# Kernel optimization log

Measured on AMD Instinct MI355X. Metric: run time of the kernel, lower is better.

## Reference

```python
import jax, jax.numpy as jnp
import numpy as np

THETA = 10000.0


def apply_rope(x, token_position, theta=THETA):
    # x: [B, H, S, d_k] with interleaved even/odd pairs; token_position: [B, S]
    B, H, S, d_k = x.shape
    inv_freq = 1.0 / theta ** (jnp.arange(0, d_k, 2, dtype=jnp.float32) / d_k)  # [d_k/2]
    angles = token_position.astype(jnp.float32)[:, :, None] * inv_freq[None, None, :]  # [B,S,d_k/2]
    cos = jnp.cos(angles)[:, None, :, :]  # [B,1,S,d_k/2]
    sin = jnp.sin(angles)[:, None, :, :]
    xp = x.reshape(B, H, S, d_k // 2, 2)
    x_even, x_odd = xp[..., 0], xp[..., 1]
    rot_even = x_even * cos - x_odd * sin
    rot_odd = x_even * sin + x_odd * cos
    return jnp.stack([rot_even, rot_odd], axis=-1).reshape(B, H, S, d_k)


def setup_inputs() -> dict:
    key = jax.random.key(0)
    ks = jax.random.split(key, 6)
    B, S, D = 2, 2048, 2048
    x = jax.random.normal(ks[0], (B, S, D), dtype=jnp.float32)
    token_position = jnp.sort(jax.random.randint(ks[1], (B, S), 0, 2048), axis=-1).astype(jnp.int32)
    scale = 0.02
    WQ = jax.random.normal(ks[2], (D, D), dtype=jnp.float32) * scale
    WK = jax.random.normal(ks[3], (D, D), dtype=jnp.float32) * scale
    WV = jax.random.normal(ks[4], (D, D), dtype=jnp.float32) * scale
    WO = jax.random.normal(ks[5], (D, D), dtype=jnp.float32) * scale
    return {"x": x, "token_position": token_position, "WQ": WQ, "WK": WK, "WV": WV, "WO": WO}


def reference(x, token_position, WQ, WK, WV, WO):
    B, S, D = x.shape
    H = 16
    d_k = D // H

    def proj(W):
        return jnp.matmul(x, W).reshape(B, S, H, d_k).transpose(0, 2, 1, 3)  # [B,H,S,d_k]

    Q = apply_rope(proj(WQ), token_position)
    K = apply_rope(proj(WK), token_position)
    V = proj(WV)

    score = jnp.einsum('bhqd,bhkd->bhqk', Q, K) / jnp.sqrt(jnp.float32(d_k))
    causal = jnp.triu(jnp.full((S, S), -jnp.inf, dtype=jnp.float32), k=1)
    score = score + causal
    attn = jax.nn.softmax(score, axis=-1)  # stable max-sub softmax, same math
    out = jnp.einsum('bhqk,bhkd->bhqd', attn, V)
    out = out.transpose(0, 2, 1, 3).reshape(B, S, D)
    return jnp.matmul(out, WO)
```

## Files before the change

kernel.cpp:

```cpp
#include <hip/hip_runtime.h>
#include <hip/hip_bf16.h>
#include <cstdint>
#include <cstddef>

typedef unsigned short u16;
typedef __attribute__((ext_vector_type(4))) unsigned short u16x4;
typedef __attribute__((ext_vector_type(8))) unsigned short u16x8;
typedef __attribute__((ext_vector_type(8))) __bf16 bf16x8;
typedef __attribute__((ext_vector_type(4))) float f32x4;

#define MFMA16(a, b, c) __builtin_amdgcn_mfma_f32_16x16x32_bf16((a), (b), (c), 0, 0, 0)

__device__ __forceinline__ u16 f2bf(float f) {
  uint32_t u = __builtin_bit_cast(uint32_t, f);
  u += 0x7FFFu + ((u >> 16) & 1u);
  return (u16)(u >> 16);
}
__device__ __forceinline__ float bf2f(u16 h) {
  return __builtin_bit_cast(float, (uint32_t)h << 16);
}

typedef const __attribute__((address_space(1))) void gv_t;
typedef __attribute__((address_space(3))) void lv_t;
__device__ __forceinline__ void gload16(const void* g, void* l) {
  __builtin_amdgcn_global_load_lds((gv_t*)g, (lv_t*)l, 16, 0, 0);
}

__global__ void cvt_f32_to_bf16(const float* __restrict__ in, u16* __restrict__ out, int n4) {
  int i = blockIdx.x * 256 + threadIdx.x;
  if (i >= n4) return;
  float4 v = ((const float4*)in)[i];
  u16x4 o;
  o[0] = f2bf(v.x); o[1] = f2bf(v.y); o[2] = f2bf(v.z); o[3] = f2bf(v.w);
  ((u16x4*)out)[i] = o;
}

__global__ void transpose_cvt4(const float* __restrict__ w0, const float* __restrict__ w1,
                               const float* __restrict__ w2, const float* __restrict__ w3,
                               u16* __restrict__ outbase) {
  __shared__ float tile[32][33];
  const int z = blockIdx.z;
  const float* in = (z == 0) ? w0 : (z == 1) ? w1 : (z == 2) ? w2 : w3;
  u16* out = outbase + (size_t)z * 4194304;
  const int bx = blockIdx.x, by = blockIdx.y;
  const int tx = threadIdx.x, ty = threadIdx.y;
#pragma unroll
  for (int i = 0; i < 32; i += 8)
    tile[ty + i][tx] = in[(size_t)(by * 32 + ty + i) * 2048 + bx * 32 + tx];
  __syncthreads();
#pragma unroll
  for (int i = 0; i < 32; i += 8)
    out[(size_t)(bx * 32 + ty + i) * 2048 + by * 32 + tx] = f2bf(tile[tx][ty + i]);
}

__global__ void vtrans(const u16* __restrict__ in, u16* __restrict__ out) {
  __shared__ u16 tile[32][34];
  const int bx = blockIdx.x, by = blockIdx.y;
  const int tx = threadIdx.x, ty = threadIdx.y;
#pragma unroll
  for (int i = 0; i < 32; i += 8)
    tile[ty + i][tx] = in[(size_t)(by * 32 + ty + i) * 2048 + bx * 32 + tx];
  __syncthreads();
#pragma unroll
  for (int i = 0; i < 32; i += 8) {
    const int c = bx * 32 + ty + i;
    const int token = by * 32 + tx;
    out[(((size_t)(token >> 11) * 16 + (c >> 7)) * 128 + (c & 127)) * 2048 + (token & 2047)] =
        tile[tx][ty + i];
  }
}

template <int MODE>
__global__ __launch_bounds__(512, 1) void gemm8(const u16* __restrict__ A,
                                                const u16* __restrict__ Bt,
                                                void* __restrict__ Cv,
                                                const int* __restrict__ pos, int nbn) {
  constexpr int K = 2048;
  __shared__ __align__(16) u16 lds[73728];
  const int tid = threadIdx.x, lane = tid & 63;
  const int lo16 = lane & 15, hi = lane >> 4;
  const int wid = tid >> 6;
  const int wr = wid >> 1, wc = wid & 1;

  const int per = (int)gridDim.x >> 3;
  const int wg = ((int)blockIdx.x & 7) * per + ((int)blockIdx.x >> 3);
  const int bn = (wg % nbn) * 128;
  const int bm = (wg / nbn) * 256;

  const int srow = tid >> 3;
  const int scol = ((tid & 7) ^ (srow & 7)) * 8;
  const u16* Arow = A + (size_t)(bm + srow) * K + scol;
  const u16* Brow = Bt + (size_t)(bn + srow) * K + scol;
  char* dstbase = (char*)lds + tid * 16;

#define STG_A(qb_, t_, r_) \
  gload16(Arow + (size_t)(r_) * 64 * K + (t_) * 64, dstbase + (qb_) * 49152 + (r_) * 8192)
#define STG_B(qb_, t_, r_) \
  gload16(Brow + (size_t)(r_) * 64 * K + (t_) * 64, dstbase + (qb_) * 49152 + 32768 + (r_) * 8192)

  f32x4 acc[4][4];
  const f32x4 z4 = {0.f, 0.f, 0.f, 0.f};
#pragma unroll
  for (int m = 0; m < 4; ++m)
#pragma unroll
    for (int n = 0; n < 4; ++n) acc[m][n] = z4;

  const int xork = lo16 & 7;
  const int aRow = (wr * 64 + lo16) * 128;
  const int bRow = 32768 + (wc * 64 + lo16) * 128;
  const int x0 = ((hi ^ xork)) << 4;
  const int x1 = (((4 + hi) ^ xork)) << 4;

  STG_A(0, 0, 0); STG_A(0, 0, 1); STG_A(0, 0, 2); STG_A(0, 0, 3);
  STG_B(0, 0, 0); STG_B(0, 0, 1);
  STG_A(1, 1, 0); STG_A(1, 1, 1); STG_A(1, 1, 2); STG_A(1, 1, 3);
  STG_B(1, 1, 0); STG_B(1, 1, 1);

  int q = 0;
  for (int t = 0; t < 32; ++t) {
    if (t < 31) {
      asm volatile("s_waitcnt vmcnt(6)" ::: "memory");
    } else {
      asm volatile("s_waitcnt vmcnt(0)" ::: "memory");
    }
    __builtin_amdgcn_s_barrier();
    __builtin_amdgcn_sched_barrier(0);
    const char* Aq = (const char*)lds + q * 49152;
    const int q2 = (q == 0) ? 2 : q - 1;

    bf16x8 a0[4], b0[4], a1[4], b1[4];
#pragma unroll
    for (int m = 0; m < 4; ++m) a0[m] = *(const bf16x8*)(Aq + aRow + m * 2048 + x0);
#pragma unroll
    for (int n = 0; n < 4; ++n) b0[n] = *(const bf16x8*)(Aq + bRow + n * 2048 + x0);
#pragma unroll
    for (int m = 0; m < 4; ++m) a1[m] = *(const bf16x8*)(Aq + aRow + m * 2048 + x1);
#pragma unroll
    for (int n = 0; n < 4; ++n) b1[n] = *(const bf16x8*)(Aq + bRow + n * 2048 + x1);

    if (t < 30) {
      STG_A(q2, t + 2, 0); STG_A(q2, t + 2, 1); STG_A(q2, t + 2, 2); STG_A(q2, t + 2, 3);
      STG_B(q2, t + 2, 0); STG_B(q2, t + 2, 1);
    }

    __builtin_amdgcn_s_setprio(1);
#pragma unroll
    for (int m = 0; m < 4; ++m)
#pragma unroll
      for (int n = 0; n < 4; ++n) acc[m][n] = MFMA16(a0[m], b0[n], acc[m][n]);
#pragma unroll
    for (int m = 0; m < 4; ++m)
#pragma unroll
      for (int n = 0; n < 4; ++n) acc[m][n] = MFMA16(a1[m], b1[n], acc[m][n]);
    __builtin_amdgcn_s_setprio(0);
    q = (q == 2) ? 0 : q + 1;
  }
#undef STG_A
#undef STG_B

  if constexpr (MODE == 2) {
    const int sect = bn >> 11;
    u16* Cq = (u16*)Cv + (size_t)sect * 8388608;
    const int cb = (bn & 2047) + wc * 64;
    if (sect < 2) {
      const float qsc = (sect == 0) ? 0.08838834764831845f : 1.0f;
      float freq[4];
#pragma unroll
      for (int n = 0; n < 4; ++n) {
        const int c = cb + n * 16 + lo16;
        freq[n] = exp2f((float)((c & 127) >> 1) * -0.2076205059304601f);
      }
      const float sg = (lo16 & 1) ? 1.f : -1.f;
#pragma unroll
      for (int m = 0; m < 4; ++m) {
        const int row = bm + wr * 64 + m * 16 + hi * 4;
#pragma unroll
        for (int r = 0; r < 4; ++r) {
          const float p = (float)pos[row + r];
#pragma unroll
          for (int n = 0; n < 4; ++n) {
            const float ang = p * freq[n];
            const float sn = __sinf(ang);
            const float cs = __cosf(ang);
            const float v = acc[m][n][r];
            const float pv = __shfl_xor(v, 1);
            Cq[(size_t)(row + r) * 2048 + cb + n * 16 + lo16] =
                f2bf((v * cs + sg * pv * sn) * qsc);
          }
        }
      }
    } else {
#pragma unroll
      for (int m = 0; m < 4; ++m)
#pragma unroll
        for (int n = 0; n < 4; ++n)
#pragma unroll
          for (int r = 0; r < 4; ++r)
            Cq[(size_t)(bm + wr * 64 + m * 16 + hi * 4 + r) * 2048 + cb + n * 16 + lo16] =
                f2bf(acc[m][n][r]);
    }
  } else {
    float* C = (float*)Cv;
    const int cb = bn + wc * 64;
#pragma unroll
    for (int m = 0; m < 4; ++m)
#pragma unroll
      for (int n = 0; n < 4; ++n)
#pragma unroll
        for (int r = 0; r < 4; ++r)
          C[(size_t)(bm + wr * 64 + m * 16 + hi * 4 + r) * 2048 + cb + n * 16 + lo16] =
              acc[m][n][r];
  }
}

__global__ __launch_bounds__(256, 2) void flash_attn4(const u16* __restrict__ Qb,
                                                      const u16* __restrict__ Kb,
                                                      const u16* __restrict__ VT,
                                                      u16* __restrict__ Ob) {
  constexpr int S = 2048, HD = 2048;
  const int g = (int)blockIdx.x;
  const int xcd = g & 7, slot = g >> 3;
  const int bh = xcd * 4 + (slot & 3);
  const int pairid = slot >> 2;
  const int b = bh >> 4, h = bh & 15;
  const int tid = threadIdx.x, lane = tid & 63, wid = tid >> 6;

  __shared__ u16 Ks[2][64 * 128];
  __shared__ u16 Vs[2][128 * 64];
  __shared__ u16 Ps[4][16 * 64];

  const size_t base = (size_t)b * S * HD + (size_t)h * 128;
  const u16* Qp = Qb + base;
  const u16* Kp = Kb + base;
  const u16* VTp = VT + (size_t)bh * 128 * S;
  u16* Op = Ob + base;

  const f32x4 z4 = {0.f, 0.f, 0.f, 0.f};
  const int kKv = (lane >> 4);
  const int kC16 = (lane & 15);
  const int vD = (lane >> 3);
  const int vC16 = (lane & 7);

#define STAGE(pb, kv0_)                                                                   \
  {                                                                                       \
    _Pragma("unroll") for (int c = 0; c < 4; ++c) {                                       \
      const int ch = wid * 4 + c;                                                         \
      {                                                                                   \
        const int kv = ch * 4 + kKv;                                                      \
        const int c16 = kC16 ^ (kv & 7);                                                  \
        gload16(Kp + (size_t)((kv0_) + kv) * HD + c16 * 8, (char*)Ks[pb] + ch * 1024);    \
      }                                                                                   \
      {                                                                                   \
        const int d = ch * 8 + vD;                                                        \
        const int c16 = vC16 ^ (d & 7);                                                   \
        gload16(VTp + (size_t)d * S + (kv0_) + c16 * 8, (char*)Vs[pb] + ch * 1024);       \
      }                                                                                   \
    }                                                                                     \
  }

#pragma unroll
  for (int half = 0; half < 2; ++half) {
    const int qt = half ? pairid : 31 - pairid;
    const int q0 = qt * 64;

    bf16x8 qf[4];
    {
      const int qr = q0 + wid * 16 + (lane & 15);
      const int kc = (lane >> 4) * 8;
#pragma unroll
      for (int kb = 0; kb < 4; ++kb)
        qf[kb] = *(const bf16x8*)(Qp + (size_t)qr * HD + kb * 32 + kc);
    }

    f32x4 accO[8];
#pragma unroll
    for (int d = 0; d < 8; ++d) accO[d] = z4;
    float m_r[4] = {-INFINITY, -INFINITY, -INFINITY, -INFINITY};
    float l_r[4] = {0.f, 0.f, 0.f, 0.f};

    STAGE(0, 0);
    __syncthreads();

    for (int t = 0; t <= qt; ++t) {
      const int cur = t & 1;
      const int kv0 = t * 64;
      if (t < qt) STAGE(cur ^ 1, kv0 + 64);

      const u16* Ksc = Ks[cur];
      const u16* Vsc = Vs[cur];
      f32x4 accS[4];
#pragma unroll
      for (int nb = 0; nb < 4; ++nb) accS[nb] = z4;

      __builtin_amdgcn_s_setprio(1);
#pragma unroll
      for (int nb = 0; nb < 4; ++nb) {
        const int kv = nb * 16 + (lane & 15);
#pragma unroll
        for (int kb = 0; kb < 4; ++kb) {
          const int c16 = (kb * 4 + (lane >> 4)) ^ (kv & 7);
          bf16x8 kf = *(const bf16x8*)((char*)Ksc + kv * 256 + c16 * 16);
          accS[nb] = MFMA16(qf[kb], kf, accS[nb]);
        }
      }
      __builtin_amdgcn_s_setprio(0);

      if (t == qt) {
#pragma unroll
        for (int nb = 0; nb < 4; ++nb) {
          const int kv = kv0 + nb * 16 + (lane & 15);
          const int qrow = q0 + wid * 16 + (lane >> 4) * 4;
#pragma unroll
          for (int j = 0; j < 4; ++j)
            if (kv > qrow + j) accS[nb][j] = -INFINITY;
        }
      }

      u16* Pw = &Ps[wid][0];
#pragma unroll
      for (int j = 0; j < 4; ++j) {
        float mx = fmaxf(fmaxf(accS[0][j], accS[1][j]), fmaxf(accS[2][j], accS[3][j]));
#pragma unroll
        for (int off = 1; off < 16; off <<= 1) mx = fmaxf(mx, __shfl_xor(mx, off));
        const float mn = fmaxf(m_r[j], mx);
        const float sc = __expf(m_r[j] - mn);
        m_r[j] = mn;
        float s = 0.f;
#pragma unroll
        for (int nb = 0; nb < 4; ++nb) {
          const float p = __expf(accS[nb][j] - mn);
          accS[nb][j] = p;
          s += p;
        }
#pragma unroll
        for (int off = 1; off < 16; off <<= 1) s += __shfl_xor(s, off);
        l_r[j] = l_r[j] * sc + s;
#pragma unroll
        for (int db = 0; db < 8; ++db) accO[db][j] *= sc;
        const int ql = (lane >> 4) * 4 + j;
#pragma unroll
        for (int nb = 0; nb < 4; ++nb) {
          const int col = nb * 16 + (lane & 15);
          const int byteoff = ql * 128 + ((((col >> 3) ^ (ql & 7))) << 4) + (col & 7) * 2;
          *(u16*)((char*)Pw + byteoff) = f2bf(accS[nb][j]);
        }
      }

#pragma unroll
      for (int kb2 = 0; kb2 < 2; ++kb2) {
        const int ql = lane & 15;
        const int c16a = (kb2 * 4 + (lane >> 4)) ^ (ql & 7);
        bf16x8 pa = *(const bf16x8*)((char*)Pw + ql * 128 + c16a * 16);
        __builtin_amdgcn_s_setprio(1);
#pragma unroll
        for (int db = 0; db < 8; ++db) {
          const int d = db * 16 + (lane & 15);
          const int c16 = (kb2 * 4 + (lane >> 4)) ^ (d & 7);
          bf16x8 vf = *(const bf16x8*)((char*)Vsc + d * 128 + c16 * 16);
          accO[db] = MFMA16(pa, vf, accO[db]);
        }
        __builtin_amdgcn_s_setprio(0);
      }
      __syncthreads();
    }

    float inv[4];
#pragma unroll
    for (int j = 0; j < 4; ++j) inv[j] = 1.f / l_r[j];
#pragma unroll
    for (int db = 0; db < 8; ++db)
#pragma unroll
      for (int j = 0; j < 4; ++j) {
        const int row = q0 + wid * 16 + (lane >> 4) * 4 + j;
        Op[(size_t)row * HD + db * 16 + (lane & 15)] = f2bf(accO[db][j] * inv[j]);
      }
  }
#undef STAGE
}

extern "C" void kernel_launch(void* const* d_in, const int* in_sizes, int n_in,
                              void* d_out, int out_size, void* d_ws, size_t ws_size,
                              hipStream_t stream) {
  const float* x  = (const float*)d_in[0];
  const int*   tp = (const int*)d_in[1];
  const float* WQ = (const float*)d_in[2];
  const float* WK = (const float*)d_in[3];
  const float* WV = (const float*)d_in[4];
  const float* WO = (const float*)d_in[5];

  const size_t MB = 1024 * 1024;
  if (ws_size < 112 * MB) return;
  char* ws = (char*)d_ws;
  u16* xb  = (u16*)(ws + 0 * MB);
  u16* wqt = (u16*)(ws + 16 * MB);
  u16* wot = (u16*)(ws + 40 * MB);
  u16* Qb  = (u16*)(ws + 48 * MB);
  u16* Kb  = (u16*)(ws + 64 * MB);
  u16* Vb  = (u16*)(ws + 80 * MB);
  u16* Obf = (u16*)(ws + 96 * MB);
  u16* VTb = xb;

  cvt_f32_to_bf16<<<8192, 256, 0, stream>>>(x, xb, 2097152);
  {
    dim3 g(64, 64, 4), blk(32, 8);
    transpose_cvt4<<<g, blk, 0, stream>>>(WQ, WK, WV, WO, wqt);
  }
  gemm8<2><<<768, 512, 0, stream>>>(xb, wqt, (void*)Qb, tp, 48);

  {
    dim3 g(64, 128), blk(32, 8);
    vtrans<<<g, blk, 0, stream>>>(Vb, VTb);
  }
  flash_attn4<<<512, 256, 0, stream>>>(Qb, Kb, VTb, Obf);

  gemm8<1><<<256, 512, 0, stream>>>(Obf, wot, d_out, nullptr, 16);
}
```

Measured before the change: 264.4 us.

## One query tile per attention block, single-buffered KV, higher occupancy; remap GEMM tiles per XCD

The attention kernel no longer pairs a long and a short query tile inside one block. It launches 1024 blocks, one query tile each, ordered longest first. The KV double buffer is removed so each block uses less LDS, and launch bounds are raised to 4 blocks per CU, letting other resident blocks hide load latency in place of in-block prefetch. The GEMM workgroup mapping now gives each XCD a contiguous range of N columns to improve L2 reuse of the weight tiles. The risk is losing in-block prefetch overlap and some tail imbalance from causal work sizes varying per block.

```diff
diff --git a/kernel.cpp b/kernel.cpp
--- a/kernel.cpp
+++ b/kernel.cpp
@@ -82,10 +82,11 @@
   const int wid = tid >> 6;
   const int wr = wid >> 1, wc = wid & 1;
 
-  const int per = (int)gridDim.x >> 3;
-  const int wg = ((int)blockIdx.x & 7) * per + ((int)blockIdx.x >> 3);
-  const int bn = (wg % nbn) * 128;
-  const int bm = (wg / nbn) * 256;
+  const int xcd = (int)blockIdx.x & 7;
+  const int idx = (int)blockIdx.x >> 3;
+  const int cpx = nbn >> 3;
+  const int bn = (xcd * cpx + idx % cpx) * 128;
+  const int bm = (idx / cpx) * 256;
 
   const int srow = tid >> 3;
   const int scol = ((tid & 7) ^ (srow & 7)) * 8;
@@ -213,7 +214,7 @@
   }
 }
 
-__global__ __launch_bounds__(256, 2) void flash_attn4(const u16* __restrict__ Qb,
+__global__ __launch_bounds__(256, 4) void flash_attn5(const u16* __restrict__ Qb,
                                                       const u16* __restrict__ Kb,
                                                       const u16* __restrict__ VT,
                                                       u16* __restrict__ Ob) {
@@ -221,12 +222,13 @@
   const int g = (int)blockIdx.x;
   const int xcd = g & 7, slot = g >> 3;
   const int bh = xcd * 4 + (slot & 3);
-  const int pairid = slot >> 2;
+  const int qt = 31 - (slot >> 2);
   const int b = bh >> 4, h = bh & 15;
   const int tid = threadIdx.x, lane = tid & 63, wid = tid >> 6;
-
-  __shared__ u16 Ks[2][64 * 128];
-  __shared__ u16 Vs[2][128 * 64];
+  const int q0 = qt * 64;
+
+  __shared__ u16 Ks[64 * 128];
+  __shared__ u16 Vs[128 * 64];
   __shared__ u16 Ps[4][16 * 64];
 
   const size_t base = (size_t)b * S * HD + (size_t)h * 128;
@@ -241,141 +243,126 @@
   const int vD = (lane >> 3);
   const int vC16 = (lane & 7);
 
-#define STAGE(pb, kv0_)                                                                   \
-  {                                                                                       \
-    _Pragma("unroll") for (int c = 0; c < 4; ++c) {                                       \
-      const int ch = wid * 4 + c;                                                         \
-      {                                                                                   \
-        const int kv = ch * 4 + kKv;                                                      \
-        const int c16 = kC16 ^ (kv & 7);                                                  \
-        gload16(Kp + (size_t)((kv0_) + kv) * HD + c16 * 8, (char*)Ks[pb] + ch * 1024);    \
-      }                                                                                   \
-      {                                                                                   \
-        const int d = ch * 8 + vD;                                                        \
-        const int c16 = vC16 ^ (d & 7);                                                   \
-        gload16(VTp + (size_t)d * S + (kv0_) + c16 * 8, (char*)Vs[pb] + ch * 1024);       \
-      }                                                                                   \
-    }                                                                                     \
-  }
-
-#pragma unroll
-  for (int half = 0; half < 2; ++half) {
-    const int qt = half ? pairid : 31 - pairid;
-    const int q0 = qt * 64;
-
-    bf16x8 qf[4];
-    {
-      const int qr = q0 + wid * 16 + (lane & 15);
-      const int kc = (lane >> 4) * 8;
-#pragma unroll
-      for (int kb = 0; kb < 4; ++kb)
-        qf[kb] = *(const bf16x8*)(Qp + (size_t)qr * HD + kb * 32 + kc);
-    }
-
-    f32x4 accO[8];
-#pragma unroll
-    for (int d = 0; d < 8; ++d) accO[d] = z4;
-    float m_r[4] = {-INFINITY, -INFINITY, -INFINITY, -INFINITY};
-    float l_r[4] = {0.f, 0.f, 0.f, 0.f};
-
-    STAGE(0, 0);
+  bf16x8 qf[4];
+  {
+    const int qr = q0 + wid * 16 + (lane & 15);
+    const int kc = (lane >> 4) * 8;
+#pragma unroll
+    for (int kb = 0; kb < 4; ++kb)
+      qf[kb] = *(const bf16x8*)(Qp + (size_t)qr * HD + kb * 32 + kc);
+  }
+
+  f32x4 accO[8];
+#pragma unroll
+  for (int d = 0; d < 8; ++d) accO[d] = z4;
+  float m_r[4] = {-INFINITY, -INFINITY, -INFINITY, -INFINITY};
+  float l_r[4] = {0.f, 0.f, 0.f, 0.f};
+
+  for (int t = 0; t <= qt; ++t) {
+    const int kv0 = t * 64;
     __syncthreads();
 
-    for (int t = 0; t <= qt; ++t) {
-      const int cur = t & 1;
-      const int kv0 = t * 64;
-      if (t < qt) STAGE(cur ^ 1, kv0 + 64);
-
-      const u16* Ksc = Ks[cur];
-      const u16* Vsc = Vs[cur];
-      f32x4 accS[4];
-#pragma unroll
-      for (int nb = 0; nb < 4; ++nb) accS[nb] = z4;
-
+#pragma unroll
+    for (int c = 0; c < 4; ++c) {
+      const int ch = wid * 4 + c;
+      {
+        const int kv = ch * 4 + kKv;
+        const int c16 = kC16 ^ (kv & 7);
+        gload16(Kp + (size_t)(kv0 + kv) * HD + c16 * 8, (char*)Ks + ch * 1024);
+      }
+      {
+        const int d = ch * 8 + vD;
+        const int c16 = vC16 ^ (d & 7);
+        gload16(VTp + (size_t)d * S + kv0 + c16 * 8, (char*)Vs + ch * 1024);
+      }
+    }
+    __syncthreads();
+
+    f32x4 accS[4];
+#pragma unroll
+    for (int nb = 0; nb < 4; ++nb) accS[nb] = z4;
+
+    __builtin_amdgcn_s_setprio(1);
+#pragma unroll
+    for (int nb = 0; nb < 4; ++nb) {
+      const int kv = nb * 16 + (lane & 15);
+#pragma unroll
+      for (int kb = 0; kb < 4; ++kb) {
+        const int c16 = (kb * 4 + (lane >> 4)) ^ (kv & 7);
+        bf16x8 kf = *(const bf16x8*)((char*)Ks + kv * 256 + c16 * 16);
+        accS[nb] = MFMA16(qf[kb], kf, accS[nb]);
+      }
+    }
+    __builtin_amdgcn_s_setprio(0);
+
+    if (t == qt) {
+#pragma unroll
+      for (int nb = 0; nb < 4; ++nb) {
+        const int kv = kv0 + nb * 16 + (lane & 15);
+        const int qrow = q0 + wid * 16 + (lane >> 4) * 4;
+#pragma unroll
+        for (int j = 0; j < 4; ++j)
+          if (kv > qrow + j) accS[nb][j] = -INFINITY;
+      }
+    }
+
+    u16* Pw = &Ps[wid][0];
+#pragma unroll
+    for (int j = 0; j < 4; ++j) {
+      float mx = fmaxf(fmaxf(accS[0][j], accS[1][j]), fmaxf(accS[2][j], accS[3][j]));
+#pragma unroll
+      for (int off = 1; off < 16; off <<= 1) mx = fmaxf(mx, __shfl_xor(mx, off));
+      const float mn = fmaxf(m_r[j], mx);
+      const float sc = __expf(m_r[j] - mn);
+      m_r[j] = mn;
+      float s = 0.f;
+#pragma unroll
+      for (int nb = 0; nb < 4; ++nb) {
+        const float p = __expf(accS[nb][j] - mn);
+        accS[nb][j] = p;
+        s += p;
+      }
+#pragma unroll
+      for (int off = 1; off < 16; off <<= 1) s += __shfl_xor(s, off);
+      l_r[j] = l_r[j] * sc + s;
+#pragma unroll
+      for (int db = 0; db < 8; ++db) accO[db][j] *= sc;
+      const int ql = (lane >> 4) * 4 + j;
+#pragma unroll
+      for (int nb = 0; nb < 4; ++nb) {
+        const int col = nb * 16 + (lane & 15);
+        const int byteoff = ql * 128 + ((((col >> 3) ^ (ql & 7))) << 4) + (col & 7) * 2;
+        *(u16*)((char*)Pw + byteoff) = f2bf(accS[nb][j]);
+      }
+    }
+
+#pragma unroll
+    for (int kb2 = 0; kb2 < 2; ++kb2) {
+      const int ql = lane & 15;
+      const int c16a = (kb2 * 4 + (lane >> 4)) ^ (ql & 7);
+      bf16x8 pa = *(const bf16x8*)((char*)Pw + ql * 128 + c16a * 16);
       __builtin_amdgcn_s_setprio(1);
 #pragma unroll
-      for (int nb = 0; nb < 4; ++nb) {
-        const int kv = nb * 16 + (lane & 15);
-#pragma unroll
-        for (int kb = 0; kb < 4; ++kb) {
-          const int c16 = (kb * 4 + (lane >> 4)) ^ (kv & 7);
-          bf16x8 kf = *(const bf16x8*)((char*)Ksc + kv * 256 + c16 * 16);
-          accS[nb] = MFMA16(qf[kb], kf, accS[nb]);
-        }
+      for (int db = 0; db < 8; ++db) {
+        const int d = db * 16 + (lane & 15);
+        const int c16 = (kb2 * 4 + (lane >> 4)) ^ (d & 7);
+        bf16x8 vf = *(const bf16x8*)((char*)Vs + d * 128 + c16 * 16);
+        accO[db] = MFMA16(pa, vf, accO[db]);
       }
       __builtin_amdgcn_s_setprio(0);
-
-      if (t == qt) {
-#pragma unroll
-        for (int nb = 0; nb < 4; ++nb) {
-          const int kv = kv0 + nb * 16 + (lane & 15);
-          const int qrow = q0 + wid * 16 + (lane >> 4) * 4;
-#pragma unroll
-          for (int j = 0; j < 4; ++j)
-            if (kv > qrow + j) accS[nb][j] = -INFINITY;
-        }
-      }
-
-      u16* Pw = &Ps[wid][0];
-#pragma unroll
-      for (int j = 0; j < 4; ++j) {
-        float mx = fmaxf(fmaxf(accS[0][j], accS[1][j]), fmaxf(accS[2][j], accS[3][j]));
-#pragma unroll
-        for (int off = 1; off < 16; off <<= 1) mx = fmaxf(mx, __shfl_xor(mx, off));
-        const float mn = fmaxf(m_r[j], mx);
-        const float sc = __expf(m_r[j] - mn);
-        m_r[j] = mn;
-        float s = 0.f;
-#pragma unroll
-        for (int nb = 0; nb < 4; ++nb) {
-          const float p = __expf(accS[nb][j] - mn);
-          accS[nb][j] = p;
-          s += p;
-        }
-#pragma unroll
-        for (int off = 1; off < 16; off <<= 1) s += __shfl_xor(s, off);
-        l_r[j] = l_r[j] * sc + s;
-#pragma unroll
-        for (int db = 0; db < 8; ++db) accO[db][j] *= sc;
-        const int ql = (lane >> 4) * 4 + j;
-#pragma unroll
-        for (int nb = 0; nb < 4; ++nb) {
-          const int col = nb * 16 + (lane & 15);
-          const int byteoff = ql * 128 + ((((col >> 3) ^ (ql & 7))) << 4) + (col & 7) * 2;
-          *(u16*)((char*)Pw + byteoff) = f2bf(accS[nb][j]);
-        }
-      }
-
-#pragma unroll
-      for (int kb2 = 0; kb2 < 2; ++kb2) {
-        const int ql = lane & 15;
-        const int c16a = (kb2 * 4 + (lane >> 4)) ^ (ql & 7);
-        bf16x8 pa = *(const bf16x8*)((char*)Pw + ql * 128 + c16a * 16);
-        __builtin_amdgcn_s_setprio(1);
-#pragma unroll
-        for (int db = 0; db < 8; ++db) {
-          const int d = db * 16 + (lane & 15);
-          const int c16 = (kb2 * 4 + (lane >> 4)) ^ (d & 7);
-          bf16x8 vf = *(const bf16x8*)((char*)Vsc + d * 128 + c16 * 16);
-          accO[db] = MFMA16(pa, vf, accO[db]);
-        }
-        __builtin_amdgcn_s_setprio(0);
-      }
-      __syncthreads();
-    }
-
-    float inv[4];
-#pragma unroll
-    for (int j = 0; j < 4; ++j) inv[j] = 1.f / l_r[j];
-#pragma unroll
-    for (int db = 0; db < 8; ++db)
-#pragma unroll
-      for (int j = 0; j < 4; ++j) {
-        const int row = q0 + wid * 16 + (lane >> 4) * 4 + j;
-        Op[(size_t)row * HD + db * 16 + (lane & 15)] = f2bf(accO[db][j] * inv[j]);
-      }
-  }
-#undef STAGE
+    }
+  }
+
+  float inv[4];
+#pragma unroll
+  for (int j = 0; j < 4; ++j) inv[j] = 1.f / l_r[j];
+#pragma unroll
+  for (int db = 0; db < 8; ++db)
+#pragma unroll
+    for (int j = 0; j < 4; ++j) {
+      const int row = q0 + wid * 16 + (lane >> 4) * 4 + j;
+      Op[(size_t)row * HD + db * 16 + (lane & 15)] = f2bf(accO[db][j] * inv[j]);
+    }
 }
 
 extern "C" void kernel_launch(void* const* d_in, const int* in_sizes, int n_in,
@@ -411,7 +398,7 @@
     dim3 g(64, 128), blk(32, 8);
     vtrans<<<g, blk, 0, stream>>>(Vb, VTb);
   }
-  flash_attn4<<<512, 256, 0, stream>>>(Qb, Kb, VTb, Obf);
+  flash_attn5<<<1024, 256, 0, stream>>>(Qb, Kb, VTb, Obf);
 
   gemm8<1><<<256, 512, 0, stream>>>(Obf, wot, d_out, nullptr, 16);
 }
```

After: 288.9 us. 1.09x slower.

## Add lazy softmax rescaling and defer row-sum reduction; remap GEMM tiles per XCD

Applied to the files above, without the earlier changes.

The attention inner loop now skips the max cross-lane reduction and accumulator rescale unless some row's new max exceeds the running max by more than 8. Per-lane partial row sums are kept and reduced across lanes only once at the end. This removes shuffles and multiplies from every KV tile. The GEMM block-to-tile mapping is also changed so each XCD gets a contiguous band of N columns, which aims at better L2 reuse. The lazy threshold lets exponentials reach about e^8 before rescaling, which stays safe in fp32 but slightly changes bf16 rounding of P.

```diff
diff --git a/kernel.cpp b/kernel.cpp
--- a/kernel.cpp
+++ b/kernel.cpp
@@ -82,10 +82,11 @@
   const int wid = tid >> 6;
   const int wr = wid >> 1, wc = wid & 1;
 
-  const int per = (int)gridDim.x >> 3;
-  const int wg = ((int)blockIdx.x & 7) * per + ((int)blockIdx.x >> 3);
-  const int bn = (wg % nbn) * 128;
-  const int bm = (wg / nbn) * 256;
+  const int xcd = (int)blockIdx.x & 7;
+  const int idx = (int)blockIdx.x >> 3;
+  const int cpx = nbn >> 3;
+  const int bn = (xcd * cpx + idx % cpx) * 128;
+  const int bm = (idx / cpx) * 256;
 
   const int srow = tid >> 3;
   const int scol = ((tid & 7) ^ (srow & 7)) * 8;
@@ -316,27 +317,38 @@
         }
       }
 
+      float lm[4];
+#pragma unroll
+      for (int j = 0; j < 4; ++j)
+        lm[j] = fmaxf(fmaxf(accS[0][j], accS[1][j]), fmaxf(accS[2][j], accS[3][j]));
+      const bool ok = (lm[0] <= m_r[0] + 8.f) && (lm[1] <= m_r[1] + 8.f) &&
+                      (lm[2] <= m_r[2] + 8.f) && (lm[3] <= m_r[3] + 8.f);
+      if (!__all(ok)) {
+#pragma unroll
+        for (int j = 0; j < 4; ++j) {
+          float mx = lm[j];
+#pragma unroll
+          for (int off = 1; off < 16; off <<= 1) mx = fmaxf(mx, __shfl_xor(mx, off));
+          const float mn = fmaxf(m_r[j], mx);
+          const float sc = __expf(m_r[j] - mn);
+          m_r[j] = mn;
+          l_r[j] *= sc;
+#pragma unroll
+          for (int db = 0; db < 8; ++db) accO[db][j] *= sc;
+        }
+      }
+
       u16* Pw = &Ps[wid][0];
 #pragma unroll
       for (int j = 0; j < 4; ++j) {
-        float mx = fmaxf(fmaxf(accS[0][j], accS[1][j]), fmaxf(accS[2][j], accS[3][j]));
-#pragma unroll
-        for (int off = 1; off < 16; off <<= 1) mx = fmaxf(mx, __shfl_xor(mx, off));
-        const float mn = fmaxf(m_r[j], mx);
-        const float sc = __expf(m_r[j] - mn);
-        m_r[j] = mn;
         float s = 0.f;
 #pragma unroll
         for (int nb = 0; nb < 4; ++nb) {
-          const float p = __expf(accS[nb][j] - mn);
+          const float p = __expf(accS[nb][j] - m_r[j]);
           accS[nb][j] = p;
           s += p;
         }
-#pragma unroll
-        for (int off = 1; off < 16; off <<= 1) s += __shfl_xor(s, off);
-        l_r[j] = l_r[j] * sc + s;
-#pragma unroll
-        for (int db = 0; db < 8; ++db) accO[db][j] *= sc;
+        l_r[j] += s;
         const int ql = (lane >> 4) * 4 + j;
 #pragma unroll
         for (int nb = 0; nb < 4; ++nb) {
@@ -366,7 +378,12 @@
 
     float inv[4];
 #pragma unroll
-    for (int j = 0; j < 4; ++j) inv[j] = 1.f / l_r[j];
+    for (int j = 0; j < 4; ++j) {
+      float l = l_r[j];
+#pragma unroll
+      for (int off = 1; off < 16; off <<= 1) l += __shfl_xor(l, off);
+      inv[j] = 1.f / l;
+    }
 #pragma unroll
     for (int db = 0; db < 8; ++db)
 #pragma unroll
```

Result: faster. 243.1 us (-8.1%).
